# Kernel tuning notes

Measured on AMD Instinct MI355X. Metric: run time of the kernel, lower is better.

The kernel has to match this reference:

```python
import jax, jax.numpy as jnp
import numpy as np

N_NODES = 50000
N_EDGES = 800000
D_IN, D_HID, D_OUT = 128, 128, 64


def setup_inputs() -> dict:
    key = jax.random.key(0)
    ks = jax.random.split(key, 10)
    return {
        "x": jax.random.normal(ks[0], (N_NODES, D_IN), dtype=jnp.float32),
        "edge_row": jax.random.randint(ks[1], (N_EDGES,), 0, N_NODES, dtype=jnp.int32),
        "edge_col": jax.random.randint(ks[2], (N_EDGES,), 0, N_NODES, dtype=jnp.int32),
        "edge_val": jax.random.uniform(ks[3], (N_EDGES,), dtype=jnp.float32),
        "W1": jax.random.normal(ks[4], (D_IN, D_HID), dtype=jnp.float32) * (1.0 / np.sqrt(D_HID)),
        "b1": jax.random.normal(ks[5], (D_HID,), dtype=jnp.float32) * (1.0 / np.sqrt(D_HID)),
        "W2": jax.random.normal(ks[6], (D_HID, D_HID), dtype=jnp.float32) * (1.0 / np.sqrt(D_HID)),
        "b2": jax.random.normal(ks[7], (D_HID,), dtype=jnp.float32) * (1.0 / np.sqrt(D_HID)),
        "W3": jax.random.normal(ks[8], (D_HID, D_OUT), dtype=jnp.float32) * (1.0 / np.sqrt(D_OUT)),
        "b3": jax.random.normal(ks[9], (D_OUT,), dtype=jnp.float32) * (1.0 / np.sqrt(D_OUT)),
    }


def _gcn_layer(x, edge_row, edge_col, edge_val, W, b):
    # support = x @ W          : dense GEMM [N, d_out]
    support = x @ W
    # spmm(adj, support)[i] = sum_e with row[e]==i: val[e] * support[col[e]]
    gathered = support[edge_col] * edge_val[:, None]  # [E, d_out]
    agg = jax.ops.segment_sum(gathered, edge_row, num_segments=x.shape[0])
    return agg + b


def reference(x, edge_row, edge_col, edge_val, W1, b1, W2, b2, W3, b3):
    # Layer 1 + ReLU (dropout is identity in eval)
    h = jax.nn.relu(_gcn_layer(x, edge_row, edge_col, edge_val, W1, b1))
    # Layer 2 + ReLU
    h = jax.nn.relu(_gcn_layer(h, edge_row, edge_col, edge_val, W2, b2))
    # Layer 3 (no activation)
    return _gcn_layer(h, edge_row, edge_col, edge_val, W3, b3)
```

## Files before the change

### kernel.cpp

```cpp
#include <hip/hip_runtime.h>

#define N_NODES 50000
#define N_EDGES 800000
#define SCAN_TILE 2048
#define CNT_STRIDE 16
#define GEMM1_BLOCKS 768
#define FUSED_BLOCKS 512
#define HIST_BLOCKS ((N_EDGES + 255) / 256)

static_assert(N_NODES < 65536, "col must fit in 16 bits for packed CSR");

typedef __attribute__((ext_vector_type(4))) float f32x4;
typedef __attribute__((ext_vector_type(8))) short bf16x8;

__device__ inline unsigned short f32_to_bf16(float f) {
    unsigned int u = __builtin_bit_cast(unsigned int, f);
    u += 0x7FFF + ((u >> 16) & 1);
    return (unsigned short)(u >> 16);
}
__device__ inline float bf16_to_f32(unsigned short h) {
    unsigned int u = ((unsigned int)h) << 16;
    return __builtin_bit_cast(float, u);
}

#define W128  (128 * 128)
#define W64   (128 * 64)
#define CNT4  (N_NODES * CNT_STRIDE / 4)

__global__ void prep(int* __restrict__ cnt, const float* __restrict__ W1,
                     const float* __restrict__ W2, const float* __restrict__ W3,
                     unsigned short* __restrict__ Wt1,
                     unsigned short* __restrict__ Wt2,
                     unsigned short* __restrict__ Wt3) {
    long long r = (long long)blockIdx.x * blockDim.x + threadIdx.x;
    if (r < CNT4) {
        int4 z = {0, 0, 0, 0};
        reinterpret_cast<int4*>(cnt)[r] = z;
        return;
    }
    r -= CNT4;
    if (r < W128) {
        int k = (int)r / 128, m = (int)r % 128;
        Wt1[m * 128 + k] = f32_to_bf16(W1[r]);
        return;
    }
    r -= W128;
    if (r < W128) {
        int k = (int)r / 128, m = (int)r % 128;
        Wt2[m * 128 + k] = f32_to_bf16(W2[r]);
        return;
    }
    r -= W128;
    if (r < W64) {
        int k = (int)r / 64, m = (int)r % 64;
        Wt3[m * 128 + k] = f32_to_bf16(W3[r]);
    }
}

template <int NOUT>
__device__ __forceinline__ void mfma_phase(const unsigned short* Xs,
                                           const unsigned short* Ws,
                                           unsigned short* __restrict__ Yb,
                                           int block_row, int N) {
    constexpr int KP = 128 + 8;
    constexpr int NT = NOUT / 16;
    const int tid = threadIdx.x;
    const int wave = tid >> 6;
    const int lane = tid & 63;
    const int m = lane & 15;
    const int quad = lane >> 4;
    const int rowbase = wave * 16;

    f32x4 acc[NT];
#pragma unroll
    for (int t = 0; t < NT; ++t) acc[t] = (f32x4){0.f, 0.f, 0.f, 0.f};

#pragma unroll
    for (int kt = 0; kt < 4; ++kt) {
        bf16x8 a = *reinterpret_cast<const bf16x8*>(
            Xs + (rowbase + m) * KP + kt * 32 + quad * 8);
#pragma unroll
        for (int t = 0; t < NT; ++t) {
            bf16x8 b = *reinterpret_cast<const bf16x8*>(
                Ws + (t * 16 + m) * KP + kt * 32 + quad * 8);
            acc[t] = __builtin_amdgcn_mfma_f32_16x16x32_bf16(a, b, acc[t], 0, 0, 0);
        }
    }

#pragma unroll
    for (int t = 0; t < NT; ++t) {
#pragma unroll
        for (int r = 0; r < 4; ++r) {
            int grow = block_row + rowbase + quad * 4 + r;
            if (grow < N)
                Yb[(size_t)grow * NOUT + t * 16 + m] = f32_to_bf16(acc[t][r]);
        }
    }
}

__global__ __launch_bounds__(256) void gemm1_hist(
    const float* __restrict__ x, const unsigned short* __restrict__ Wt,
    unsigned short* __restrict__ Yb, int N, int ntiles,
    const int* __restrict__ erow, int* __restrict__ cnt, int* __restrict__ rank) {
    constexpr int KP = 128 + 8;
    __shared__ unsigned short Xs[64 * KP];
    __shared__ unsigned short Ws[128 * KP];
    const int tid = threadIdx.x;

    if (blockIdx.x >= GEMM1_BLOCKS) {
        int e = (blockIdx.x - GEMM1_BLOCKS) * blockDim.x + tid;
        if (e < N_EDGES) rank[e] = atomicAdd(&cnt[(size_t)erow[e] * CNT_STRIDE], 1);
        return;
    }

    for (int idx = tid; idx < 128 * 16; idx += 256) {
        int r = idx >> 4, ch = idx & 15;
        uint4 v = *reinterpret_cast<const uint4*>(Wt + r * 128 + ch * 8);
        *reinterpret_cast<uint4*>(Ws + r * KP + ch * 8) = v;
    }

    for (int tile = blockIdx.x; tile < ntiles; tile += GEMM1_BLOCKS) {
        const int block_row = tile * 64;
        for (int idx = tid; idx < 64 * 16; idx += 256) {
            int r = idx >> 4, ch = idx & 15;
            int gr = block_row + r;
            if (gr >= N) gr = N - 1;
            const float4* xp =
                reinterpret_cast<const float4*>(x + (size_t)gr * 128 + ch * 8);
            float4 a = xp[0], b = xp[1];
            uint4 o;
            o.x = (unsigned int)f32_to_bf16(a.x) | ((unsigned int)f32_to_bf16(a.y) << 16);
            o.y = (unsigned int)f32_to_bf16(a.z) | ((unsigned int)f32_to_bf16(a.w) << 16);
            o.z = (unsigned int)f32_to_bf16(b.x) | ((unsigned int)f32_to_bf16(b.y) << 16);
            o.w = (unsigned int)f32_to_bf16(b.z) | ((unsigned int)f32_to_bf16(b.w) << 16);
            *reinterpret_cast<uint4*>(Xs + r * KP + ch * 8) = o;
        }
        __syncthreads();
        mfma_phase<128>(Xs, Ws, Yb, block_row, N);
        __syncthreads();
    }
}

__global__ void scan_fused(const int* __restrict__ cnt, int* __restrict__ tsum,
                           int* __restrict__ done, int* __restrict__ rptr,
                           int n, int ntiles) {
    __shared__ int sums[256];
    __shared__ int off_s;
    const int t = threadIdx.x;
    const int b = blockIdx.x;
    const int base = b * SCAN_TILE + t * 8;
    int v[8], pref[8];
    int s = 0;
#pragma unroll
    for (int i = 0; i < 8; ++i) {
        v[i] = (base + i < n) ? cnt[(size_t)(base + i) * CNT_STRIDE] : 0;
        s += v[i];
    }
    sums[t] = s;
    __syncthreads();
    for (int off = 1; off < 256; off <<= 1) {
        int x = (t >= off) ? sums[t - off] : 0;
        __syncthreads();
        sums[t] += x;
        __syncthreads();
    }
    int run = sums[t] - s;
#pragma unroll
    for (int i = 0; i < 8; ++i) {
        pref[i] = run;
        run += v[i];
    }
    if (t == 255) {
        tsum[b] = run;
        __threadfence();
        atomicAdd(done, 1);
    }
    if (t == 0) {
        while (__hip_atomic_load(done, __ATOMIC_ACQUIRE, __HIP_MEMORY_SCOPE_AGENT) <
               ntiles) {
        }
        __threadfence();
        int off = 0;
        for (int i = 0; i < b; ++i) off += tsum[i];
        off_s = off;
        if (b == 0) {
            int tot = 0;
            for (int i = 0; i < ntiles; ++i) tot += tsum[i];
            rptr[n] = tot;
        }
    }
    __syncthreads();
    const int off = off_s;
#pragma unroll
    for (int i = 0; i < 8; ++i) {
        int idx = base + i;
        if (idx < n) rptr[idx] = pref[i] + off;
    }
}

__global__ void fill_csr(const int* __restrict__ erow, const int* __restrict__ ecol,
                         const float* __restrict__ eval, const int* __restrict__ rptr,
                         const int* __restrict__ rank,
                         unsigned int* __restrict__ cpack) {
    int e = blockIdx.x * blockDim.x + threadIdx.x;
    if (e >= N_EDGES) return;
    int slot = rptr[erow[e]] + rank[e];
    unsigned int p = (unsigned int)(ecol[e] & 0xFFFF) |
                     ((unsigned int)f32_to_bf16(eval[e]) << 16);
    cpack[slot] = p;
}

template <int NOUT>
__device__ __forceinline__ void mfma_phase512(const unsigned short* Xs,
                                              const unsigned short* Ws,
                                              unsigned short* __restrict__ Yb,
                                              int block_row, int N) {
    constexpr int KP = 128 + 8;
    constexpr int NT = NOUT / 16;
    constexpr int NTH = NT / 2;
    const int tid = threadIdx.x;
    const int wave = tid >> 6;
    const int lane = tid & 63;
    const int m = lane & 15;
    const int quad = lane >> 4;
    const int rowbase = (wave & 3) * 16;
    const int tbase = (wave >> 2) * NTH;

    f32x4 acc[NTH];
#pragma unroll
    for (int t = 0; t < NTH; ++t) acc[t] = (f32x4){0.f, 0.f, 0.f, 0.f};

#pragma unroll
    for (int kt = 0; kt < 4; ++kt) {
        bf16x8 a = *reinterpret_cast<const bf16x8*>(
            Xs + (rowbase + m) * KP + kt * 32 + quad * 8);
#pragma unroll
        for (int t = 0; t < NTH; ++t) {
            bf16x8 b = *reinterpret_cast<const bf16x8*>(
                Ws + ((tbase + t) * 16 + m) * KP + kt * 32 + quad * 8);
            acc[t] = __builtin_amdgcn_mfma_f32_16x16x32_bf16(a, b, acc[t], 0, 0, 0);
        }
    }

#pragma unroll
    for (int t = 0; t < NTH; ++t) {
#pragma unroll
        for (int r = 0; r < 4; ++r) {
            int grow = block_row + rowbase + quad * 4 + r;
            if (grow < N)
                Yb[(size_t)grow * NOUT + (tbase + t) * 16 + m] = f32_to_bf16(acc[t][r]);
        }
    }
}

template <int NOUT>
__global__ __launch_bounds__(512, 4) void gemm_fused_agg(
    const unsigned short* __restrict__ S,
    const int* __restrict__ rptr, const unsigned int* __restrict__ cpack,
    const float* __restrict__ bias,
    const unsigned short* __restrict__ Wt,
    unsigned short* __restrict__ Yb,
    int N, int ntiles) {
    constexpr int KP = 128 + 8;
    __shared__ unsigned short Xs[64 * KP];
    __shared__ unsigned short Ws[NOUT * KP];
    const int tid = threadIdx.x;
    const int group = tid >> 4;
    const int f8 = tid & 15;

    for (int idx = tid; idx < NOUT * 16; idx += 512) {
        int r = idx >> 4, ch = idx & 15;
        uint4 v = *reinterpret_cast<const uint4*>(Wt + r * 128 + ch * 8);
        *reinterpret_cast<uint4*>(Ws + r * KP + ch * 8) = v;
    }

    float bv[8];
#pragma unroll
    for (int i = 0; i < 8; ++i) bv[i] = bias[f8 * 8 + i];

    for (int tile = blockIdx.x; tile < ntiles; tile += gridDim.x) {
        const int block_row = tile * 64;
#pragma unroll
        for (int r4 = 0; r4 < 2; ++r4) {
            const int row = r4 * 32 + group;
            const int node = block_row + row;
            float acc[8];
#pragma unroll
            for (int i = 0; i < 8; ++i) acc[i] = bv[i];
            if (node < N) {
                const int beg = rptr[node];
                const int end = rptr[node + 1];
                int j = beg;
                for (; j + 8 <= end; j += 8) {
                    unsigned int p[8];
                    uint4 s[8];
#pragma unroll
                    for (int u = 0; u < 8; ++u) p[u] = cpack[j + u];
#pragma unroll
                    for (int u = 0; u < 8; ++u)
                        s[u] = *reinterpret_cast<const uint4*>(
                            S + (size_t)(p[u] & 0xFFFF) * 128 + f8 * 8);
#pragma unroll
                    for (int u = 0; u < 8; ++u) {
                        const float v = bf16_to_f32((unsigned short)(p[u] >> 16));
                        const unsigned short* sp =
                            reinterpret_cast<const unsigned short*>(&s[u]);
#pragma unroll
                        for (int i = 0; i < 8; ++i)
                            acc[i] = fmaf(v, bf16_to_f32(sp[i]), acc[i]);
                    }
                }
                if (j + 4 <= end) {
                    unsigned int p[4];
                    uint4 s[4];
#pragma unroll
                    for (int u = 0; u < 4; ++u) p[u] = cpack[j + u];
#pragma unroll
                    for (int u = 0; u < 4; ++u)
                        s[u] = *reinterpret_cast<const uint4*>(
                            S + (size_t)(p[u] & 0xFFFF) * 128 + f8 * 8);
#pragma unroll
                    for (int u = 0; u < 4; ++u) {
                        const float v = bf16_to_f32((unsigned short)(p[u] >> 16));
                        const unsigned short* sp =
                            reinterpret_cast<const unsigned short*>(&s[u]);
#pragma unroll
                        for (int i = 0; i < 8; ++i)
                            acc[i] = fmaf(v, bf16_to_f32(sp[i]), acc[i]);
                    }
                    j += 4;
                }
                if (j + 2 <= end) {
                    unsigned int p[2];
                    uint4 s[2];
#pragma unroll
                    for (int u = 0; u < 2; ++u) p[u] = cpack[j + u];
#pragma unroll
                    for (int u = 0; u < 2; ++u)
                        s[u] = *reinterpret_cast<const uint4*>(
                            S + (size_t)(p[u] & 0xFFFF) * 128 + f8 * 8);
#pragma unroll
                    for (int u = 0; u < 2; ++u) {
                        const float v = bf16_to_f32((unsigned short)(p[u] >> 16));
                        const unsigned short* sp =
                            reinterpret_cast<const unsigned short*>(&s[u]);
#pragma unroll
                        for (int i = 0; i < 8; ++i)
                            acc[i] = fmaf(v, bf16_to_f32(sp[i]), acc[i]);
                    }
                    j += 2;
                }
                if (j < end) {
                    unsigned int p = cpack[j];
                    uint4 s = *reinterpret_cast<const uint4*>(
                        S + (size_t)(p & 0xFFFF) * 128 + f8 * 8);
                    const float v = bf16_to_f32((unsigned short)(p >> 16));
                    const unsigned short* sp =
                        reinterpret_cast<const unsigned short*>(&s);
#pragma unroll
                    for (int i = 0; i < 8; ++i)
                        acc[i] = fmaf(v, bf16_to_f32(sp[i]), acc[i]);
                }
            }
            uint4 o;
            o.x = (unsigned int)f32_to_bf16(fmaxf(acc[0], 0.f)) |
                  ((unsigned int)f32_to_bf16(fmaxf(acc[1], 0.f)) << 16);
            o.y = (unsigned int)f32_to_bf16(fmaxf(acc[2], 0.f)) |
                  ((unsigned int)f32_to_bf16(fmaxf(acc[3], 0.f)) << 16);
            o.z = (unsigned int)f32_to_bf16(fmaxf(acc[4], 0.f)) |
                  ((unsigned int)f32_to_bf16(fmaxf(acc[5], 0.f)) << 16);
            o.w = (unsigned int)f32_to_bf16(fmaxf(acc[6], 0.f)) |
                  ((unsigned int)f32_to_bf16(fmaxf(acc[7], 0.f)) << 16);
            *reinterpret_cast<uint4*>(Xs + row * KP + f8 * 8) = o;
        }
        __syncthreads();
        mfma_phase512<NOUT>(Xs, Ws, Yb, block_row, N);
        __syncthreads();
    }
}

__global__ void aggregate_bf16_64(const unsigned short* __restrict__ S,
                                  const int* __restrict__ rptr,
                                  const unsigned int* __restrict__ cpack,
                                  const float* __restrict__ bias,
                                  float* __restrict__ out, int N) {
    const int node = blockIdx.x * (blockDim.x / 8) + threadIdx.x / 8;
    const int f8 = threadIdx.x & 7;
    if (node >= N) return;
    const int beg = rptr[node];
    const int end = rptr[node + 1];
    float acc[8];
#pragma unroll
    for (int i = 0; i < 8; ++i) acc[i] = bias[f8 * 8 + i];
    int j = beg;
    for (; j + 8 <= end; j += 8) {
        unsigned int p[8];
        uint4 s[8];
#pragma unroll
        for (int u = 0; u < 8; ++u) p[u] = cpack[j + u];
#pragma unroll
        for (int u = 0; u < 8; ++u)
            s[u] = *reinterpret_cast<const uint4*>(S + (size_t)(p[u] & 0xFFFF) * 64 + f8 * 8);
#pragma unroll
        for (int u = 0; u < 8; ++u) {
            const float v = bf16_to_f32((unsigned short)(p[u] >> 16));
            const unsigned short* sp = reinterpret_cast<const unsigned short*>(&s[u]);
#pragma unroll
            for (int i = 0; i < 8; ++i) acc[i] = fmaf(v, bf16_to_f32(sp[i]), acc[i]);
        }
    }
    if (j + 4 <= end) {
        unsigned int p[4];
        uint4 s[4];
#pragma unroll
        for (int u = 0; u < 4; ++u) p[u] = cpack[j + u];
#pragma unroll
        for (int u = 0; u < 4; ++u)
            s[u] = *reinterpret_cast<const uint4*>(S + (size_t)(p[u] & 0xFFFF) * 64 + f8 * 8);
#pragma unroll
        for (int u = 0; u < 4; ++u) {
            const float v = bf16_to_f32((unsigned short)(p[u] >> 16));
            const unsigned short* sp = reinterpret_cast<const unsigned short*>(&s[u]);
#pragma unroll
            for (int i = 0; i < 8; ++i) acc[i] = fmaf(v, bf16_to_f32(sp[i]), acc[i]);
        }
        j += 4;
    }
    if (j + 2 <= end) {
        unsigned int p[2];
        uint4 s[2];
#pragma unroll
        for (int u = 0; u < 2; ++u) p[u] = cpack[j + u];
#pragma unroll
        for (int u = 0; u < 2; ++u)
            s[u] = *reinterpret_cast<const uint4*>(S + (size_t)(p[u] & 0xFFFF) * 64 + f8 * 8);
#pragma unroll
        for (int u = 0; u < 2; ++u) {
            const float v = bf16_to_f32((unsigned short)(p[u] >> 16));
            const unsigned short* sp = reinterpret_cast<const unsigned short*>(&s[u]);
#pragma unroll
            for (int i = 0; i < 8; ++i) acc[i] = fmaf(v, bf16_to_f32(sp[i]), acc[i]);
        }
        j += 2;
    }
    if (j < end) {
        unsigned int p = cpack[j];
        uint4 s = *reinterpret_cast<const uint4*>(S + (size_t)(p & 0xFFFF) * 64 + f8 * 8);
        const float v = bf16_to_f32((unsigned short)(p >> 16));
        const unsigned short* sp = reinterpret_cast<const unsigned short*>(&s);
#pragma unroll
        for (int i = 0; i < 8; ++i) acc[i] = fmaf(v, bf16_to_f32(sp[i]), acc[i]);
    }
    float4 o0 = {acc[0], acc[1], acc[2], acc[3]};
    float4 o1 = {acc[4], acc[5], acc[6], acc[7]};
    float* op = out + (size_t)node * 64 + f8 * 8;
    *reinterpret_cast<float4*>(op) = o0;
    *reinterpret_cast<float4*>(op + 4) = o1;
}

extern "C" void kernel_launch(void* const* d_in, const int* in_sizes, int n_in,
                              void* d_out, int out_size, void* d_ws, size_t ws_size,
                              hipStream_t stream) {
    const float* x    = (const float*)d_in[0];
    const int*   erow = (const int*)d_in[1];
    const int*   ecol = (const int*)d_in[2];
    const float* eval = (const float*)d_in[3];
    const float* W1   = (const float*)d_in[4];
    const float* b1   = (const float*)d_in[5];
    const float* W2   = (const float*)d_in[6];
    const float* b2   = (const float*)d_in[7];
    const float* W3   = (const float*)d_in[8];
    const float* b3   = (const float*)d_in[9];
    float* out = (float*)d_out;

    const size_t nf = (size_t)N_NODES * 128;
    unsigned short* SA  = (unsigned short*)d_ws;
    unsigned short* SB  = SA + nf;
    unsigned short* Wt1 = SB + nf;
    unsigned short* Wt2 = Wt1 + 128 * 128;
    unsigned short* Wt3 = Wt2 + 128 * 128;
    int*   cnt    = (int*)(Wt3 + 64 * 128);
    int*   rank   = cnt + (size_t)N_NODES * CNT_STRIDE;
    int*   rptr   = rank + N_EDGES;
    unsigned int* cpack = (unsigned int*)(rptr + N_NODES + 1);
    int*   stsum  = (int*)(cpack + N_EDGES);
    int*   done   = cnt + 1;

    const int blk = 256;
    const int ntiles_g = (N_NODES + 63) / 64;
    const int agg_grid = (int)(((long long)N_NODES * 8 + blk - 1) / blk);
    const int ntiles = (N_NODES + SCAN_TILE - 1) / SCAN_TILE;

    {
        long long total = (long long)CNT4 + W128 + W128 + W64;
        prep<<<(int)((total + blk - 1) / blk), blk, 0, stream>>>(
            cnt, W1, W2, W3, Wt1, Wt2, Wt3);
    }

    gemm1_hist<<<GEMM1_BLOCKS + HIST_BLOCKS, 256, 0, stream>>>(
        x, Wt1, SA, N_NODES, ntiles_g, erow, cnt, rank);

    scan_fused<<<ntiles, 256, 0, stream>>>(cnt, stsum, done, rptr, N_NODES, ntiles);

    fill_csr<<<HIST_BLOCKS, blk, 0, stream>>>(erow, ecol, eval, rptr, rank, cpack);

    gemm_fused_agg<128><<<FUSED_BLOCKS, 512, 0, stream>>>(
        SA, rptr, cpack, b1, Wt2, SB, N_NODES, ntiles_g);

    gemm_fused_agg<64><<<FUSED_BLOCKS, 512, 0, stream>>>(
        SB, rptr, cpack, b2, Wt3, SA, N_NODES, ntiles_g);

    aggregate_bf16_64<<<agg_grid, blk, 0, stream>>>(SA, rptr, cpack, b3, out, N_NODES);
}
```

Measured before the change: 231.6 us.

## Privatize degree histogram per XCD with XCD-local atomics

Replaces the single padded per-node counter array with one counter array per XCD, read from the hardware XCC id register. Atomics are issued with the sc0 (XCD-local) scope, and the XCD id is packed into the high bits of the rank. The scan sums the eight partial counts per node and writes per-XCD offsets that fill_csr uses to place each edge. This aims to avoid cross-die coherent atomics in the histogram, at the cost of more scan reads and writes and reliance on the XCD-local atomic actually being coherent within one die.

Result: slower. 247.1 us (+6.7%).

```diff
diff --git a/kernel.cpp b/kernel.cpp
--- a/kernel.cpp
+++ b/kernel.cpp
@@ -3,7 +3,7 @@
 #define N_NODES 50000
 #define N_EDGES 800000
 #define SCAN_TILE 2048
-#define CNT_STRIDE 16
+#define N_XCD 8
 #define GEMM1_BLOCKS 768
 #define FUSED_BLOCKS 512
 #define HIST_BLOCKS ((N_EDGES + 255) / 256)
@@ -23,9 +23,27 @@
     return __builtin_bit_cast(float, u);
 }
 
+__device__ inline int get_xcc_id() {
+    int x;
+    asm volatile("s_getreg_b32 %0, hwreg(20, 0, 32)" : "=s"(x));
+    return x & (N_XCD - 1);
+}
+
+__device__ inline int atomic_add_xcd_local(int* p, int v) {
+    int old;
+    asm volatile(
+        "global_atomic_add %0, %1, %2, off sc0\n\t"
+        "s_waitcnt vmcnt(0)"
+        : "=v"(old)
+        : "v"(p), "v"(v)
+        : "memory");
+    return old;
+}
+
 #define W128  (128 * 128)
 #define W64   (128 * 64)
-#define CNT4  (N_NODES * CNT_STRIDE / 4)
+#define CNT_INTS (N_XCD * N_NODES + 4)
+#define CNT4  (CNT_INTS / 4)
 
 __global__ void prep(int* __restrict__ cnt, const float* __restrict__ W1,
                      const float* __restrict__ W2, const float* __restrict__ W3,
@@ -109,7 +127,12 @@
 
     if (blockIdx.x >= GEMM1_BLOCKS) {
         int e = (blockIdx.x - GEMM1_BLOCKS) * blockDim.x + tid;
-        if (e < N_EDGES) rank[e] = atomicAdd(&cnt[(size_t)erow[e] * CNT_STRIDE], 1);
+        if (e < N_EDGES) {
+            const int xcc = get_xcc_id();
+            int old = atomic_add_xcd_local(
+                &cnt[(size_t)xcc * N_NODES + erow[e]], 1);
+            rank[e] = (xcc << 27) | old;
+        }
         return;
     }
 
@@ -143,7 +166,7 @@
 
 __global__ void scan_fused(const int* __restrict__ cnt, int* __restrict__ tsum,
                            int* __restrict__ done, int* __restrict__ rptr,
-                           int n, int ntiles) {
+                           int* __restrict__ xoff, int n, int ntiles) {
     __shared__ int sums[256];
     __shared__ int off_s;
     const int t = threadIdx.x;
@@ -153,8 +176,14 @@
     int s = 0;
 #pragma unroll
     for (int i = 0; i < 8; ++i) {
-        v[i] = (base + i < n) ? cnt[(size_t)(base + i) * CNT_STRIDE] : 0;
-        s += v[i];
+        int d = 0;
+        if (base + i < n) {
+#pragma unroll
+            for (int r = 0; r < N_XCD; ++r)
+                d += cnt[(size_t)r * N_NODES + base + i];
+        }
+        v[i] = d;
+        s += d;
     }
     sums[t] = s;
     __syncthreads();
@@ -194,17 +223,26 @@
 #pragma unroll
     for (int i = 0; i < 8; ++i) {
         int idx = base + i;
-        if (idx < n) rptr[idx] = pref[i] + off;
+        if (idx < n) {
+            int rb = pref[i] + off;
+            rptr[idx] = rb;
+#pragma unroll
+            for (int r = 0; r < N_XCD; ++r) {
+                xoff[(size_t)r * N_NODES + idx] = rb;
+                rb += cnt[(size_t)r * N_NODES + idx];
+            }
+        }
     }
 }
 
 __global__ void fill_csr(const int* __restrict__ erow, const int* __restrict__ ecol,
-                         const float* __restrict__ eval, const int* __restrict__ rptr,
+                         const float* __restrict__ eval, const int* __restrict__ xoff,
                          const int* __restrict__ rank,
                          unsigned int* __restrict__ cpack) {
     int e = blockIdx.x * blockDim.x + threadIdx.x;
     if (e >= N_EDGES) return;
-    int slot = rptr[erow[e]] + rank[e];
+    int rk = rank[e];
+    int slot = xoff[(size_t)(rk >> 27) * N_NODES + erow[e]] + (rk & 0x07FFFFFF);
     unsigned int p = (unsigned int)(ecol[e] & 0xFFFF) |
                      ((unsigned int)f32_to_bf16(eval[e]) << 16);
     cpack[slot] = p;
@@ -480,11 +518,12 @@
     unsigned short* Wt2 = Wt1 + 128 * 128;
     unsigned short* Wt3 = Wt2 + 128 * 128;
     int*   cnt    = (int*)(Wt3 + 64 * 128);
-    int*   rank   = cnt + (size_t)N_NODES * CNT_STRIDE;
+    int*   rank   = cnt + CNT_INTS;
     int*   rptr   = rank + N_EDGES;
-    unsigned int* cpack = (unsigned int*)(rptr + N_NODES + 1);
+    int*   xoff   = rptr + (N_NODES + 1);
+    unsigned int* cpack = (unsigned int*)(xoff + (size_t)N_XCD * N_NODES);
     int*   stsum  = (int*)(cpack + N_EDGES);
-    int*   done   = cnt + 1;
+    int*   done   = cnt + N_XCD * N_NODES;
 
     const int blk = 256;
     const int ntiles_g = (N_NODES + 63) / 64;
@@ -500,9 +539,10 @@
     gemm1_hist<<<GEMM1_BLOCKS + HIST_BLOCKS, 256, 0, stream>>>(
         x, Wt1, SA, N_NODES, ntiles_g, erow, cnt, rank);
 
-    scan_fused<<<ntiles, 256, 0, stream>>>(cnt, stsum, done, rptr, N_NODES, ntiles);
-
-    fill_csr<<<HIST_BLOCKS, blk, 0, stream>>>(erow, ecol, eval, rptr, rank, cpack);
+    scan_fused<<<ntiles, 256, 0, stream>>>(cnt, stsum, done, rptr, xoff,
+                                           N_NODES, ntiles);
+
+    fill_csr<<<HIST_BLOCKS, blk, 0, stream>>>(erow, ecol, eval, xoff, rank, cpack);
 
     gemm_fused_agg<128><<<FUSED_BLOCKS, 512, 0, stream>>>(
         SA, rptr, cpack, b1, Wt2, SB, N_NODES, ntiles_g);
```

## Replace global atomic row histogram with per-block LDS histograms and bases

Applied to the files above, without the earlier changes.

Row counting moves out of the GEMM1 kernel into 64 blocks. Each block builds a packed 16-bit histogram in shared memory with LDS atomics, which removes the zeroing of a strided global count array and the 800k global atomics. The scan then sums the 64 per-block histograms and writes a per-block base offset table, which fill_csr uses to place edges. The cost is extra global traffic for the histogram and base tables, a scan with long sequential per-thread loops over only a few blocks, and no more overlap of the histogram with GEMM1.

Result: slower. 236.3 us (+2.0%).

```diff
diff --git a/kernel.cpp b/kernel.cpp
--- a/kernel.cpp
+++ b/kernel.cpp
@@ -3,12 +3,19 @@
 #define N_NODES 50000
 #define N_EDGES 800000
 #define SCAN_TILE 2048
-#define CNT_STRIDE 16
 #define GEMM1_BLOCKS 768
 #define FUSED_BLOCKS 512
-#define HIST_BLOCKS ((N_EDGES + 255) / 256)
+#define FILL_BLOCKS ((N_EDGES + 255) / 256)
+
+#define HB 64
+#define EPB (N_EDGES / HB)
+#define HGROUPS (EPB / 4)
+#define HHALF (N_NODES / 2)
+#define HHALF4 (HHALF / 4)
 
 static_assert(N_NODES < 65536, "col must fit in 16 bits for packed CSR");
+static_assert(N_EDGES % (4 * HB) == 0, "chunking must be exact");
+static_assert(EPB < 65536, "packed u16 counts must not overflow");
 
 typedef __attribute__((ext_vector_type(4))) float f32x4;
 typedef __attribute__((ext_vector_type(8))) short bf16x8;
@@ -25,20 +32,50 @@
 
 #define W128  (128 * 128)
 #define W64   (128 * 64)
-#define CNT4  (N_NODES * CNT_STRIDE / 4)
-
-__global__ void prep(int* __restrict__ cnt, const float* __restrict__ W1,
-                     const float* __restrict__ W2, const float* __restrict__ W3,
-                     unsigned short* __restrict__ Wt1,
-                     unsigned short* __restrict__ Wt2,
-                     unsigned short* __restrict__ Wt3) {
-    long long r = (long long)blockIdx.x * blockDim.x + threadIdx.x;
-    if (r < CNT4) {
-        int4 z = {0, 0, 0, 0};
-        reinterpret_cast<int4*>(cnt)[r] = z;
+
+__global__ __launch_bounds__(256) void prep_hist(
+    const int* __restrict__ erow, int* __restrict__ rank,
+    int* __restrict__ bhist, int* __restrict__ done_,
+    const float* __restrict__ W1, const float* __restrict__ W2,
+    const float* __restrict__ W3,
+    unsigned short* __restrict__ Wt1, unsigned short* __restrict__ Wt2,
+    unsigned short* __restrict__ Wt3) {
+    __shared__ int h[HHALF];
+    const int tid = threadIdx.x;
+    if (blockIdx.x < HB) {
+        const int b = blockIdx.x;
+        int4* h4 = reinterpret_cast<int4*>(h);
+        for (int i = tid; i < HHALF4; i += 256) {
+            int4 z = {0, 0, 0, 0};
+            h4[i] = z;
+        }
+        __syncthreads();
+        const int4* eg = reinterpret_cast<const int4*>(erow) + (size_t)b * HGROUPS;
+        int4* rg = reinterpret_cast<int4*>(rank) + (size_t)b * HGROUPS;
+        for (int g = tid; g < HGROUPS; g += 256) {
+            int4 er = eg[g];
+            int4 rk;
+            int sh, o;
+            sh = (er.x & 1) << 4;
+            o = atomicAdd(&h[er.x >> 1], 1 << sh);
+            rk.x = (o >> sh) & 0xFFFF;
+            sh = (er.y & 1) << 4;
+            o = atomicAdd(&h[er.y >> 1], 1 << sh);
+            rk.y = (o >> sh) & 0xFFFF;
+            sh = (er.z & 1) << 4;
+            o = atomicAdd(&h[er.z >> 1], 1 << sh);
+            rk.z = (o >> sh) & 0xFFFF;
+            sh = (er.w & 1) << 4;
+            o = atomicAdd(&h[er.w >> 1], 1 << sh);
+            rk.w = (o >> sh) & 0xFFFF;
+            rg[g] = rk;
+        }
+        __syncthreads();
+        int4* dst = reinterpret_cast<int4*>(bhist + (size_t)b * HHALF);
+        for (int i = tid; i < HHALF4; i += 256) dst[i] = h4[i];
         return;
     }
-    r -= CNT4;
+    long long r = (long long)(blockIdx.x - HB) * 256 + tid;
     if (r < W128) {
         int k = (int)r / 128, m = (int)r % 128;
         Wt1[m * 128 + k] = f32_to_bf16(W1[r]);
@@ -54,7 +91,10 @@
     if (r < W64) {
         int k = (int)r / 64, m = (int)r % 64;
         Wt3[m * 128 + k] = f32_to_bf16(W3[r]);
-    }
+        return;
+    }
+    r -= W64;
+    if (r == 0) *done_ = 0;
 }
 
 template <int NOUT>
@@ -98,20 +138,13 @@
     }
 }
 
-__global__ __launch_bounds__(256) void gemm1_hist(
+__global__ __launch_bounds__(256) void gemm1(
     const float* __restrict__ x, const unsigned short* __restrict__ Wt,
-    unsigned short* __restrict__ Yb, int N, int ntiles,
-    const int* __restrict__ erow, int* __restrict__ cnt, int* __restrict__ rank) {
+    unsigned short* __restrict__ Yb, int N, int ntiles) {
     constexpr int KP = 128 + 8;
     __shared__ unsigned short Xs[64 * KP];
     __shared__ unsigned short Ws[128 * KP];
     const int tid = threadIdx.x;
-
-    if (blockIdx.x >= GEMM1_BLOCKS) {
-        int e = (blockIdx.x - GEMM1_BLOCKS) * blockDim.x + tid;
-        if (e < N_EDGES) rank[e] = atomicAdd(&cnt[(size_t)erow[e] * CNT_STRIDE], 1);
-        return;
-    }
 
     for (int idx = tid; idx < 128 * 16; idx += 256) {
         int r = idx >> 4, ch = idx & 15;
@@ -141,21 +174,31 @@
     }
 }
 
-__global__ void scan_fused(const int* __restrict__ cnt, int* __restrict__ tsum,
+__global__ void scan_fused(const int* __restrict__ bhist, int* __restrict__ tsum,
                            int* __restrict__ done, int* __restrict__ rptr,
-                           int n, int ntiles) {
+                           int* __restrict__ bbase, int n, int ntiles) {
     __shared__ int sums[256];
     __shared__ int off_s;
     const int t = threadIdx.x;
     const int b = blockIdx.x;
     const int base = b * SCAN_TILE + t * 8;
+    const int nidx = base >> 3;
+    const int4* bh4 = reinterpret_cast<const int4*>(bhist);
     int v[8], pref[8];
+#pragma unroll
+    for (int i = 0; i < 8; ++i) v[i] = 0;
+    if (base < n) {
+        for (int hb = 0; hb < HB; ++hb) {
+            int4 p = bh4[hb * HHALF4 + nidx];
+            v[0] += p.x & 0xFFFF; v[1] += (int)((unsigned)p.x >> 16);
+            v[2] += p.y & 0xFFFF; v[3] += (int)((unsigned)p.y >> 16);
+            v[4] += p.z & 0xFFFF; v[5] += (int)((unsigned)p.z >> 16);
+            v[6] += p.w & 0xFFFF; v[7] += (int)((unsigned)p.w >> 16);
+        }
+    }
     int s = 0;
 #pragma unroll
-    for (int i = 0; i < 8; ++i) {
-        v[i] = (base + i < n) ? cnt[(size_t)(base + i) * CNT_STRIDE] : 0;
-        s += v[i];
-    }
+    for (int i = 0; i < 8; ++i) s += v[i];
     sums[t] = s;
     __syncthreads();
     for (int off = 1; off < 256; off <<= 1) {
@@ -191,20 +234,36 @@
     }
     __syncthreads();
     const int off = off_s;
-#pragma unroll
-    for (int i = 0; i < 8; ++i) {
-        int idx = base + i;
-        if (idx < n) rptr[idx] = pref[i] + off;
+    if (base < n) {
+        int rn[8];
+#pragma unroll
+        for (int i = 0; i < 8; ++i) rn[i] = pref[i] + off;
+        int4 r0 = {rn[0], rn[1], rn[2], rn[3]};
+        int4 r1 = {rn[4], rn[5], rn[6], rn[7]};
+        *reinterpret_cast<int4*>(rptr + base) = r0;
+        *reinterpret_cast<int4*>(rptr + base + 4) = r1;
+        for (int hb = 0; hb < HB; ++hb) {
+            int4 p = bh4[hb * HHALF4 + nidx];
+            int4 o0 = {rn[0], rn[1], rn[2], rn[3]};
+            int4 o1 = {rn[4], rn[5], rn[6], rn[7]};
+            int4* bb = reinterpret_cast<int4*>(bbase + (size_t)hb * N_NODES + base);
+            bb[0] = o0;
+            bb[1] = o1;
+            rn[0] += p.x & 0xFFFF; rn[1] += (int)((unsigned)p.x >> 16);
+            rn[2] += p.y & 0xFFFF; rn[3] += (int)((unsigned)p.y >> 16);
+            rn[4] += p.z & 0xFFFF; rn[5] += (int)((unsigned)p.z >> 16);
+            rn[6] += p.w & 0xFFFF; rn[7] += (int)((unsigned)p.w >> 16);
+        }
     }
 }
 
 __global__ void fill_csr(const int* __restrict__ erow, const int* __restrict__ ecol,
-                         const float* __restrict__ eval, const int* __restrict__ rptr,
+                         const float* __restrict__ eval, const int* __restrict__ bbase,
                          const int* __restrict__ rank,
                          unsigned int* __restrict__ cpack) {
     int e = blockIdx.x * blockDim.x + threadIdx.x;
     if (e >= N_EDGES) return;
-    int slot = rptr[erow[e]] + rank[e];
+    int slot = bbase[(size_t)(e / EPB) * N_NODES + erow[e]] + rank[e];
     unsigned int p = (unsigned int)(ecol[e] & 0xFFFF) |
                      ((unsigned int)f32_to_bf16(eval[e]) << 16);
     cpack[slot] = p;
@@ -479,12 +538,13 @@
     unsigned short* Wt1 = SB + nf;
     unsigned short* Wt2 = Wt1 + 128 * 128;
     unsigned short* Wt3 = Wt2 + 128 * 128;
-    int*   cnt    = (int*)(Wt3 + 64 * 128);
-    int*   rank   = cnt + (size_t)N_NODES * CNT_STRIDE;
-    int*   rptr   = rank + N_EDGES;
+    int*   rank   = (int*)(Wt3 + 64 * 128);
+    int*   bhist  = rank + N_EDGES;
+    int*   bbase  = bhist + (size_t)HB * HHALF;
+    int*   rptr   = bbase + (size_t)HB * N_NODES;
     unsigned int* cpack = (unsigned int*)(rptr + N_NODES + 1);
     int*   stsum  = (int*)(cpack + N_EDGES);
-    int*   done   = cnt + 1;
+    int*   done   = stsum + 32;
 
     const int blk = 256;
     const int ntiles_g = (N_NODES + 63) / 64;
@@ -492,17 +552,18 @@
     const int ntiles = (N_NODES + SCAN_TILE - 1) / SCAN_TILE;
 
     {
-        long long total = (long long)CNT4 + W128 + W128 + W64;
-        prep<<<(int)((total + blk - 1) / blk), blk, 0, stream>>>(
-            cnt, W1, W2, W3, Wt1, Wt2, Wt3);
-    }
-
-    gemm1_hist<<<GEMM1_BLOCKS + HIST_BLOCKS, 256, 0, stream>>>(
-        x, Wt1, SA, N_NODES, ntiles_g, erow, cnt, rank);
-
-    scan_fused<<<ntiles, 256, 0, stream>>>(cnt, stsum, done, rptr, N_NODES, ntiles);
-
-    fill_csr<<<HIST_BLOCKS, blk, 0, stream>>>(erow, ecol, eval, rptr, rank, cpack);
+        long long wtotal = (long long)W128 + W128 + W64 + 1;
+        int wblocks = (int)((wtotal + blk - 1) / blk);
+        prep_hist<<<HB + wblocks, blk, 0, stream>>>(
+            erow, rank, bhist, done, W1, W2, W3, Wt1, Wt2, Wt3);
+    }
+
+    gemm1<<<GEMM1_BLOCKS, 256, 0, stream>>>(x, Wt1, SA, N_NODES, ntiles_g);
+
+    scan_fused<<<ntiles, 256, 0, stream>>>(bhist, stsum, done, rptr, bbase,
+                                           N_NODES, ntiles);
+
+    fill_csr<<<FILL_BLOCKS, blk, 0, stream>>>(erow, ecol, eval, bbase, rank, cpack);
 
     gemm_fused_agg<128><<<FUSED_BLOCKS, 512, 0, stream>>>(
         SA, rptr, cpack, b1, Wt2, SB, N_NODES, ntiles_g);
```
